# Optimization experiments

Measured on AMD Instinct MI355X. Metric: run time of the kernel, lower is better.

Reference implementation:

```python
import jax, jax.numpy as jnp
import numpy as np

HIDDEN = 2048
N_HEADS = 16
N_KV_HEADS = 8
HEAD_DIM = 128
ROTARY_DIM = 32  # int(128 * 0.25), already even
ROPE_THETA = 10000000.0
EPS = 1e-6
BATCH, SEQ = 2, 2048


def _rmsnorm(x, w, eps=EPS):
    # per-head RMSNorm over last dim; weight is zero-init, scale = 1 + w
    r = jax.lax.rsqrt(jnp.mean(x * x, axis=-1, keepdims=True) + eps)
    return x * r * (1.0 + w)


def _rope(x, positions, rotary_dim, theta):
    # x: [b, s, h, rotary_dim]; rotate-halves RoPE
    half = rotary_dim // 2
    inv_freq = 1.0 / (theta ** (jnp.arange(half, dtype=jnp.float32) / half))
    ang = positions.astype(jnp.float32)[:, :, None] * inv_freq  # [b, s, half]
    cos = jnp.cos(ang)[:, :, None, :]
    sin = jnp.sin(ang)[:, :, None, :]
    x1, x2 = x[..., :half], x[..., half:]
    return jnp.concatenate([x1 * cos - x2 * sin, x1 * sin + x2 * cos], axis=-1)


def setup_inputs() -> dict:
    key = jax.random.key(0)
    ks = jax.random.split(key, 8)
    scale = lambda fan_in: 1.0 / np.sqrt(fan_in)
    x = jax.random.normal(ks[0], (BATCH, SEQ, HIDDEN), dtype=jnp.float32)
    Wq = jax.random.normal(ks[1], (HIDDEN, N_HEADS * HEAD_DIM * 2), jnp.float32) * scale(HIDDEN)
    Wk = jax.random.normal(ks[2], (HIDDEN, N_KV_HEADS * HEAD_DIM), jnp.float32) * scale(HIDDEN)
    Wv = jax.random.normal(ks[3], (HIDDEN, N_KV_HEADS * HEAD_DIM), jnp.float32) * scale(HIDDEN)
    Wo = jax.random.normal(ks[4], (N_HEADS * HEAD_DIM, HIDDEN), jnp.float32) * scale(N_HEADS * HEAD_DIM)
    q_norm_w = jax.random.normal(ks[5], (HEAD_DIM,), jnp.float32) * 0.02
    k_norm_w = jax.random.normal(ks[6], (HEAD_DIM,), jnp.float32) * 0.02
    attention_mask = jnp.ones((BATCH, SEQ), dtype=jnp.int32)
    positions = jnp.broadcast_to(jnp.arange(SEQ, dtype=jnp.int32), (BATCH, SEQ))
    return {"x": x, "attention_mask": attention_mask, "positions": positions,
            "Wq": Wq, "Wk": Wk, "Wv": Wv, "Wo": Wo,
            "q_norm_w": q_norm_w, "k_norm_w": k_norm_w}


def reference(x, attention_mask, positions, Wq, Wk, Wv, Wo, q_norm_w, k_norm_w):
    b, s, _ = x.shape
    g = N_HEADS // N_KV_HEADS  # GQA group size

    q_all = jnp.einsum('bsh,ho->bso', x, Wq).reshape(b, s, N_HEADS, HEAD_DIM * 2)
    q, gate = jnp.split(q_all, 2, axis=-1)          # each [b,s,H,D]
    gate = gate.reshape(b, s, N_HEADS * HEAD_DIM)
    q = _rmsnorm(q, q_norm_w)
    k = _rmsnorm(jnp.einsum('bsh,ho->bso', x, Wk).reshape(b, s, N_KV_HEADS, HEAD_DIM), k_norm_w)
    v = jnp.einsum('bsh,ho->bso', x, Wv).reshape(b, s, N_KV_HEADS, HEAD_DIM)

    # partial RoPE on first ROTARY_DIM dims
    q = jnp.concatenate([_rope(q[..., :ROTARY_DIM], positions, ROTARY_DIM, ROPE_THETA), q[..., ROTARY_DIM:]], axis=-1)
    k = jnp.concatenate([_rope(k[..., :ROTARY_DIM], positions, ROTARY_DIM, ROPE_THETA), k[..., ROTARY_DIM:]], axis=-1)

    # grouped-query causal attention
    qg = q.reshape(b, s, N_KV_HEADS, g, HEAD_DIM)
    scores = jnp.einsum('bqhgd,bkhd->bhgqk', qg, k) / jnp.sqrt(jnp.float32(HEAD_DIM))
    causal = jnp.tril(jnp.ones((s, s), dtype=bool))
    key_valid = attention_mask.astype(bool)[:, None, None, None, :]  # [b,1,1,1,k]
    mask = causal[None, None, None, :, :] & key_valid
    scores = jnp.where(mask, scores, jnp.finfo(scores.dtype).min)
    probs = jax.nn.softmax(scores, axis=-1)
    attn = jnp.einsum('bhgqk,bkhd->bqhgd', probs, v).reshape(b, s, N_HEADS * HEAD_DIM)

    attn = attn * jax.nn.sigmoid(gate)
    return jnp.einsum('bso,oh->bsh', attn, Wo)
```

## Files before the change

### kernel.cpp

```cpp
#include <hip/hip_runtime.h>
#include <cstdint>

typedef __bf16  bf16;
typedef __bf16  bf16x8 __attribute__((ext_vector_type(8)));
typedef __bf16  bf16x4 __attribute__((ext_vector_type(4)));
typedef __bf16  bf16x2 __attribute__((ext_vector_type(2)));
typedef float   f32x4  __attribute__((ext_vector_type(4)));
typedef float   f32x16 __attribute__((ext_vector_type(16)));

#define GLOAD_LDS16(g, l) __builtin_amdgcn_global_load_lds( \
    (const __attribute__((address_space(1))) void*)(g),     \
    (__attribute__((address_space(3))) void*)(l), 16, 0, 0)

#define SEQ   2048
#define HID   2048
#define NH    16
#define NKV   8
#define HD    128
#define NQKV  6144
#define MTOT  4096

__device__ __forceinline__ void transw_body(const float* __restrict__ W, bf16* __restrict__ WT,
                                            int N, int n0, int k0, int t) {
    __shared__ float tile[64][65];
    int tn = t & 63, t4 = t >> 6;
    #pragma unroll
    for (int i = 0; i < 16; ++i) {
        int kk = i * 4 + t4;
        tile[kk][tn] = W[(size_t)(k0 + kk) * N + n0 + tn];
    }
    __syncthreads();
    #pragma unroll
    for (int i = 0; i < 16; ++i) {
        int nn = i * 4 + t4;
        WT[(size_t)(n0 + nn) * HID + k0 + tn] = (bf16)tile[tn][nn];
    }
}

__global__ __launch_bounds__(256) void prep_kernel(const float* __restrict__ x, bf16* __restrict__ xb,
                                                   const float* __restrict__ Wq, const float* __restrict__ Wk,
                                                   const float* __restrict__ Wv, const float* __restrict__ Wo,
                                                   bf16* __restrict__ wqkvT, bf16* __restrict__ woT) {
    int bx = blockIdx.x, t = threadIdx.x;
    if (bx < 8192) {
        int i = bx * 256 + t;
        f32x4 v = ((const f32x4*)x)[i];
        bf16x4 o;
        o[0] = (bf16)v[0]; o[1] = (bf16)v[1]; o[2] = (bf16)v[2]; o[3] = (bf16)v[3];
        ((bf16x4*)xb)[i] = o;
    } else if (bx < 8192 + 2048) {
        int idx = bx - 8192;
        transw_body(Wq, wqkvT, 4096, (idx & 63) * 64, (idx >> 6) * 64, t);
    } else if (bx < 8192 + 2048 + 512) {
        int idx = bx - (8192 + 2048);
        transw_body(Wk, wqkvT + (size_t)4096 * HID, 1024, (idx & 15) * 64, (idx >> 4) * 64, t);
    } else if (bx < 8192 + 2048 + 1024) {
        int idx = bx - (8192 + 2048 + 512);
        transw_body(Wv, wqkvT + (size_t)5120 * HID, 1024, (idx & 15) * 64, (idx >> 4) * 64, t);
    } else {
        int idx = bx - (8192 + 2048 + 1024);
        transw_body(Wo, woT, 2048, (idx & 31) * 64, (idx >> 5) * 64, t);
    }
}

template<bool OUT_BF16>
__global__ __launch_bounds__(256) void gemm_bt(const bf16* __restrict__ A, const bf16* __restrict__ Bt,
                                               void* __restrict__ C, int M, int N, int K) {
    __shared__ __align__(16) bf16 As[128 * 64];
    __shared__ __align__(16) bf16 Bs[128 * 64];
    const int tid = threadIdx.x;
    const int wave = tid >> 6, lane = tid & 63;
    const int l31 = lane & 31, half = lane >> 5;
    const int tile_n = blockIdx.x * 128, tile_m = blockIdx.y * 128;
    const int wm = (wave & 1) * 64, wn = (wave >> 1) * 64;
    const int sw = l31 & 7;
    f32x16 acc[2][2] = {};

    for (int k0 = 0; k0 < K; k0 += 64) {
        __syncthreads();
        #pragma unroll
        for (int j = 0; j < 4; ++j) {
            int s = j * 256 + tid;
            int row = s >> 3, c = s & 7;
            int cs = c ^ (row & 7);
            GLOAD_LDS16(A  + (size_t)(tile_m + row) * K + k0 + (cs << 3), As + (size_t)s * 8);
            GLOAD_LDS16(Bt + (size_t)(tile_n + row) * K + k0 + (cs << 3), Bs + (size_t)s * 8);
        }
        __syncthreads();
        #pragma unroll
        for (int ks = 0; ks < 4; ++ks) {
            int ch = ((ks * 2 + half) ^ sw) << 3;
            bf16x8 a0 = *(const bf16x8*)(As + (size_t)(wm + l31) * 64 + ch);
            bf16x8 a1 = *(const bf16x8*)(As + (size_t)(wm + 32 + l31) * 64 + ch);
            bf16x8 b0 = *(const bf16x8*)(Bs + (size_t)(wn + l31) * 64 + ch);
            bf16x8 b1 = *(const bf16x8*)(Bs + (size_t)(wn + 32 + l31) * 64 + ch);
            acc[0][0] = __builtin_amdgcn_mfma_f32_32x32x16_bf16(a0, b0, acc[0][0], 0, 0, 0);
            acc[0][1] = __builtin_amdgcn_mfma_f32_32x32x16_bf16(a0, b1, acc[0][1], 0, 0, 0);
            acc[1][0] = __builtin_amdgcn_mfma_f32_32x32x16_bf16(a1, b0, acc[1][0], 0, 0, 0);
            acc[1][1] = __builtin_amdgcn_mfma_f32_32x32x16_bf16(a1, b1, acc[1][1], 0, 0, 0);
        }
    }
    #pragma unroll
    for (int mt = 0; mt < 2; ++mt)
        #pragma unroll
        for (int nt = 0; nt < 2; ++nt)
            #pragma unroll
            for (int reg = 0; reg < 16; ++reg) {
                int row = tile_m + wm + mt * 32 + (reg & 3) + ((reg >> 2) * 8) + half * 4;
                int col = tile_n + wn + nt * 32 + l31;
                float v = acc[mt][nt][reg];
                if (OUT_BF16) ((bf16*)C)[(size_t)row * N + col] = (bf16)v;
                else          ((float*)C)[(size_t)row * N + col] = v;
            }
}

__global__ __launch_bounds__(256) void post_kernel(const bf16* __restrict__ qkv,
                                                   const float* __restrict__ qnw, const float* __restrict__ knw,
                                                   const int* __restrict__ positions,
                                                   bf16* __restrict__ Qh, bf16* __restrict__ Kh,
                                                   bf16* __restrict__ VT) {
    int bx = blockIdx.x;
    if (bx < 4096) {
        int tk = bx;
        int b = tk >> 11, s = tk & 2047;
        int wave = threadIdx.x >> 6, lane = threadIdx.x & 63;
        int e0 = lane * 2, e1 = e0 + 1;
        float pos = (float)positions[tk];
        const float L = 1.4533435415278355f;
        float a0 = pos * exp2f(-(float)(e0 & 15) * L);
        float a1 = pos * exp2f(-(float)(e1 & 15) * L);
        float cv0 = cosf(a0), sv0 = sinf(a0);
        float cv1 = cosf(a1), sv1 = sinf(a1);
        float qw0 = 1.0f + qnw[e0], qw1 = 1.0f + qnw[e1];
        float kw0 = 1.0f + knw[e0], kw1 = 1.0f + knw[e1];

        #pragma unroll
        for (int i = 0; i < 6; ++i) {
            bool isq = (i < 4);
            int h = wave + (isq ? i : (i - 4)) * 4;
            const bf16* base = qkv + (size_t)tk * NQKV + (isq ? h * 256 : 4096 + h * HD);
            bf16x2 v = *(const bf16x2*)(base + e0);
            float f0 = (float)v[0], f1 = (float)v[1];
            float ssq = f0 * f0 + f1 * f1;
            #pragma unroll
            for (int off = 32; off; off >>= 1) ssq += __shfl_xor(ssq, off);
            float rn = rsqrtf(ssq * (1.0f / 128.0f) + 1e-6f);
            float w0 = isq ? qw0 : kw0, w1 = isq ? qw1 : kw1;
            float x0 = f0 * rn * w0, x1 = f1 * rn * w1;
            float p0 = __shfl_xor(x0, 8), p1 = __shfl_xor(x1, 8);
            float r0 = x0, r1 = x1;
            if (lane < 8)       { r0 = x0 * cv0 - p0 * sv0; r1 = x1 * cv1 - p1 * sv1; }
            else if (lane < 16) { r0 = p0 * sv0 + x0 * cv0; r1 = p1 * sv1 + x1 * cv1; }
            bf16x2 o; o[0] = (bf16)r0; o[1] = (bf16)r1;
            bf16* dst = isq ? (Qh + ((size_t)(b * NH + h) * SEQ + s) * HD)
                            : (Kh + ((size_t)(b * NKV + h) * SEQ + s) * HD);
            *(bf16x2*)(dst + e0) = o;
        }
    } else {
        int idx = bx - 4096;
        int bh = idx >> 5, st = idx & 31;
        int b = bh >> 3, h = bh & 7;
        __shared__ float tile[64][129];
        int t = threadIdx.x;
        const bf16* src = qkv + ((size_t)(b * SEQ) + st * 64) * NQKV + 5120 + h * HD;
        #pragma unroll
        for (int i = 0; i < 32; ++i) {
            int ii = i * 256 + t;
            int tok = ii >> 7, d = ii & 127;
            tile[tok][d] = (float)src[(size_t)tok * NQKV + d];
        }
        __syncthreads();
        bf16* dst = VT + (size_t)(b * NKV + h) * HD * SEQ + st * 64;
        #pragma unroll
        for (int i = 0; i < 32; ++i) {
            int ii = i * 256 + t;
            int d = ii >> 6, sx = ii & 63;
            dst[(size_t)d * SEQ + sx] = (bf16)tile[sx][d];
        }
    }
}

__global__ __launch_bounds__(512, 4) void attn_kernel(const bf16* __restrict__ Qh, const bf16* __restrict__ Kh,
                                                      const bf16* __restrict__ VT, const bf16* __restrict__ qkv,
                                                      const int* __restrict__ amask, bf16* __restrict__ attnb) {
    const int bx = blockIdx.x;
    const int hb = (bx >> 4) & 31;
    const int head = hb & 15, b = hb >> 4;
    int q0 = ((bx & 15) + hb) & 15;
    const int qt = (bx & 256) ? (15 - q0) : q0;
    const int kvh = head >> 1;
    __shared__ __align__(16) bf16 Ks[2][64 * 128];
    __shared__ __align__(16) bf16 Vs[2][128 * 64];
    __shared__ __align__(16) bf16 Ps[8 * 16 * 64];
    const int tid = threadIdx.x, wave = tid >> 6, lane = tid & 63;
    const int quad = lane >> 4, cl = lane & 15;

    const bf16* qsrc = Qh + ((size_t)(b * NH + head) * SEQ + qt * 128) * HD;
    bf16x8 aq[4];
    #pragma unroll
    for (int kc = 0; kc < 4; ++kc)
        aq[kc] = *(const bf16x8*)(qsrc + (size_t)(wave * 16 + cl) * HD + kc * 32 + quad * 8);

    float lstate[4] = {0.0f, 0.0f, 0.0f, 0.0f};
    f32x4 oacc[8] = {};
    const int qrow_glob = qt * 128 + wave * 16 + quad * 4;
    const float scale = 0.08838834764831845f * 1.4426950408889634f;
    const float M = 20.0f;
    const int kmax = 2 * qt + 1;

    const bf16* kbase = Kh + (size_t)(b * NKV + kvh) * SEQ * HD;
    const bf16* vbase = VT + (size_t)(b * NKV + kvh) * HD * SEQ;

#define STAGE_KV(kt_, buf_) { \
    const bf16* ksrc = kbase + (size_t)(kt_) * 64 * HD; \
    const bf16* vsrc = vbase + (size_t)(kt_) * 64; \
    _Pragma("unroll") \
    for (int j = 0; j < 2; ++j) { \
        int s = j * 512 + tid;                     \
        int rK = s >> 4, cK = s & 15; \
        GLOAD_LDS16(ksrc + (size_t)rK * HD + ((cK ^ (rK & 15)) << 3), &Ks[buf_][0] + (size_t)s * 8); \
        int dV = s >> 3, cV = s & 7; \
        GLOAD_LDS16(vsrc + (size_t)dV * SEQ + ((cV ^ (dV & 7)) << 3), &Vs[buf_][0] + (size_t)s * 8); \
    } }

    STAGE_KV(0, 0);
    int cur = 0;
    for (int kt = 0; kt <= kmax; ++kt) {
        __syncthreads();
        if (kt < kmax) STAGE_KV(kt + 1, cur ^ 1);

        f32x4 sc[4] = {};
        #pragma unroll
        for (int nt = 0; nt < 4; ++nt)
            #pragma unroll
            for (int kc = 0; kc < 4; ++kc) {
                bf16x8 bk = *(const bf16x8*)(&Ks[cur][0] + (size_t)(nt * 16 + cl) * 128 + (((kc * 4 + quad) ^ cl) << 3));
                sc[nt] = __builtin_amdgcn_mfma_f32_16x16x32_bf16(aq[kc], bk, sc[nt], 0, 0, 0);
            }

        #pragma unroll
        for (int nt = 0; nt < 4; ++nt) {
            int kcol = kt * 64 + nt * 16 + cl;
            bool cok = (amask[b * SEQ + kcol] != 0);
            #pragma unroll
            for (int r = 0; r < 4; ++r) {
                bool ok = cok && (kcol <= qrow_glob + r);
                float p = ok ? exp2f(sc[nt][r] * scale - M) : 0.0f;
                lstate[r] += p;
                Ps[wave * 1024 + (quad * 4 + r) * 64 + ((nt * 16 + cl) ^ (quad << 4))] = (bf16)p;
            }
        }

        bf16x8 ap[2];
        #pragma unroll
        for (int c = 0; c < 2; ++c)
            ap[c] = *(const bf16x8*)(Ps + wave * 1024 + cl * 64 + ((c * 32 + quad * 8) ^ ((cl >> 2) << 4)));
        #pragma unroll
        for (int n2 = 0; n2 < 8; ++n2)
            #pragma unroll
            for (int c = 0; c < 2; ++c) {
                bf16x8 bv = *(const bf16x8*)(&Vs[cur][0] + (size_t)(n2 * 16 + cl) * 64 + (((c * 4 + quad) ^ (cl & 7)) << 3));
                oacc[n2] = __builtin_amdgcn_mfma_f32_16x16x32_bf16(ap[c], bv, oacc[n2], 0, 0, 0);
            }
        cur ^= 1;
    }
#undef STAGE_KV

    #pragma unroll
    for (int r = 0; r < 4; ++r) {
        #pragma unroll
        for (int off = 8; off; off >>= 1) lstate[r] += __shfl_xor(lstate[r], off);
        int srow = qt * 128 + wave * 16 + quad * 4 + r;
        float linv = 1.0f / lstate[r];
        #pragma unroll
        for (int n2 = 0; n2 < 8; ++n2) {
            int d = n2 * 16 + cl;
            float g = (float)qkv[(size_t)(b * SEQ + srow) * NQKV + head * 256 + 128 + d];
            float sig = 1.0f / (1.0f + __expf(-g));
            float v = oacc[n2][r] * linv * sig;
            attnb[(size_t)(b * SEQ + srow) * HID + head * HD + d] = (bf16)v;
        }
    }
}

extern "C" void kernel_launch(void* const* d_in, const int* in_sizes, int n_in,
                              void* d_out, int out_size, void* d_ws, size_t ws_size,
                              hipStream_t stream) {
    const float* x        = (const float*)d_in[0];
    const int*   amask    = (const int*)d_in[1];
    const int*   positions= (const int*)d_in[2];
    const float* Wq       = (const float*)d_in[3];
    const float* Wk       = (const float*)d_in[4];
    const float* Wv       = (const float*)d_in[5];
    const float* Wo       = (const float*)d_in[6];
    const float* qnw      = (const float*)d_in[7];
    const float* knw      = (const float*)d_in[8];
    float* out = (float*)d_out;
    char* ws = (char*)d_ws;

    bf16* xb    = (bf16*)(ws);
    bf16* wqkvT = (bf16*)(ws + 16777216);
    bf16* woT   = (bf16*)(ws + 41943040);
    bf16* qkv   = (bf16*)(ws + 50331648);
    bf16* Qh    = (bf16*)(ws + 100663296);
    bf16* Kh    = (bf16*)(ws + 117440512);
    bf16* VT    = (bf16*)(ws + 125829120);
    bf16* attnb = (bf16*)(ws + 134217728);

    prep_kernel<<<12288, 256, 0, stream>>>(x, xb, Wq, Wk, Wv, Wo, wqkvT, woT);
    gemm_bt<true><<<dim3(48, 32), 256, 0, stream>>>(xb, wqkvT, qkv, MTOT, NQKV, HID);
    post_kernel<<<4608, 256, 0, stream>>>(qkv, qnw, knw, positions, Qh, Kh, VT);
    attn_kernel<<<512, 512, 0, stream>>>(Qh, Kh, VT, qkv, amask, attnb);
    gemm_bt<false><<<dim3(16, 32), 256, 0, stream>>>(attnb, woT, out, MTOT, HID, HID);

    (void)in_sizes; (void)n_in; (void)out_size; (void)ws_size;
}
```

Baseline: 390.5 us.

## Vectorize prep/post memory accesses and ballot the attention mask per tile

The weight transpose now writes 16-byte bf16x8 vectors instead of scalar bf16 stores. The x conversion handles eight elements per thread with half the blocks. The post kernel processes eight elements per lane and reads the norm weights as vectors, computing RoPE sin/cos only on rotary lanes. The attention kernel loads the mask once per key tile and distributes it with a ballot, replacing a per-column global load. These cut instruction count and memory transactions in the bandwidth-bound auxiliary kernels, at the cost of more LDS bank conflicts in the strided transpose reads.

```diff
diff --git a/kernel.cpp b/kernel.cpp
--- a/kernel.cpp
+++ b/kernel.cpp
@@ -30,10 +30,15 @@
         tile[kk][tn] = W[(size_t)(k0 + kk) * N + n0 + tn];
     }
     __syncthreads();
-    #pragma unroll
-    for (int i = 0; i < 16; ++i) {
-        int nn = i * 4 + t4;
-        WT[(size_t)(n0 + nn) * HID + k0 + tn] = (bf16)tile[tn][nn];
+    int tk8 = (t & 7) * 8;
+    int tnn = t >> 3;
+    #pragma unroll
+    for (int i = 0; i < 2; ++i) {
+        int nn = i * 32 + tnn;
+        bf16x8 o;
+        #pragma unroll
+        for (int j = 0; j < 8; ++j) o[j] = (bf16)tile[tk8 + j][nn];
+        *(bf16x8*)(&WT[(size_t)(n0 + nn) * HID + k0 + tk8]) = o;
     }
 }
 
@@ -42,23 +47,25 @@
                                                    const float* __restrict__ Wv, const float* __restrict__ Wo,
                                                    bf16* __restrict__ wqkvT, bf16* __restrict__ woT) {
     int bx = blockIdx.x, t = threadIdx.x;
-    if (bx < 8192) {
+    if (bx < 4096) {
         int i = bx * 256 + t;
-        f32x4 v = ((const f32x4*)x)[i];
-        bf16x4 o;
-        o[0] = (bf16)v[0]; o[1] = (bf16)v[1]; o[2] = (bf16)v[2]; o[3] = (bf16)v[3];
-        ((bf16x4*)xb)[i] = o;
-    } else if (bx < 8192 + 2048) {
-        int idx = bx - 8192;
+        f32x4 v0 = ((const f32x4*)x)[i * 2];
+        f32x4 v1 = ((const f32x4*)x)[i * 2 + 1];
+        bf16x8 o;
+        o[0] = (bf16)v0[0]; o[1] = (bf16)v0[1]; o[2] = (bf16)v0[2]; o[3] = (bf16)v0[3];
+        o[4] = (bf16)v1[0]; o[5] = (bf16)v1[1]; o[6] = (bf16)v1[2]; o[7] = (bf16)v1[3];
+        ((bf16x8*)xb)[i] = o;
+    } else if (bx < 4096 + 2048) {
+        int idx = bx - 4096;
         transw_body(Wq, wqkvT, 4096, (idx & 63) * 64, (idx >> 6) * 64, t);
-    } else if (bx < 8192 + 2048 + 512) {
-        int idx = bx - (8192 + 2048);
+    } else if (bx < 4096 + 2048 + 512) {
+        int idx = bx - (4096 + 2048);
         transw_body(Wk, wqkvT + (size_t)4096 * HID, 1024, (idx & 15) * 64, (idx >> 4) * 64, t);
-    } else if (bx < 8192 + 2048 + 1024) {
-        int idx = bx - (8192 + 2048 + 512);
+    } else if (bx < 4096 + 2048 + 1024) {
+        int idx = bx - (4096 + 2048 + 512);
         transw_body(Wv, wqkvT + (size_t)5120 * HID, 1024, (idx & 15) * 64, (idx >> 4) * 64, t);
     } else {
-        int idx = bx - (8192 + 2048 + 1024);
+        int idx = bx - (4096 + 2048 + 1024);
         transw_body(Wo, woT, 2048, (idx & 31) * 64, (idx >> 5) * 64, t);
     }
 }
@@ -124,37 +131,59 @@
         int tk = bx;
         int b = tk >> 11, s = tk & 2047;
         int wave = threadIdx.x >> 6, lane = threadIdx.x & 63;
-        int e0 = lane * 2, e1 = e0 + 1;
+        int g16 = lane >> 4;
+        int l16 = lane & 15;
+        int d0 = l16 * 8;
         float pos = (float)positions[tk];
         const float L = 1.4533435415278355f;
-        float a0 = pos * exp2f(-(float)(e0 & 15) * L);
-        float a1 = pos * exp2f(-(float)(e1 & 15) * L);
-        float cv0 = cosf(a0), sv0 = sinf(a0);
-        float cv1 = cosf(a1), sv1 = sinf(a1);
-        float qw0 = 1.0f + qnw[e0], qw1 = 1.0f + qnw[e1];
-        float kw0 = 1.0f + knw[e0], kw1 = 1.0f + knw[e1];
-
-        #pragma unroll
-        for (int i = 0; i < 6; ++i) {
-            bool isq = (i < 4);
-            int h = wave + (isq ? i : (i - 4)) * 4;
-            const bf16* base = qkv + (size_t)tk * NQKV + (isq ? h * 256 : 4096 + h * HD);
-            bf16x2 v = *(const bf16x2*)(base + e0);
-            float f0 = (float)v[0], f1 = (float)v[1];
-            float ssq = f0 * f0 + f1 * f1;
-            #pragma unroll
-            for (int off = 32; off; off >>= 1) ssq += __shfl_xor(ssq, off);
+
+        float cv[8], sv[8];
+        if (l16 < 4) {
+            #pragma unroll
+            for (int j = 0; j < 8; ++j) {
+                float a = pos * exp2f(-(float)((l16 & 1) * 8 + j) * L);
+                cv[j] = cosf(a); sv[j] = sinf(a);
+            }
+        }
+
+        #pragma unroll
+        for (int i = 0; i < 2; ++i) {
+            int slot = i * 16 + wave * 4 + g16;
+            if (slot >= 24) continue;
+            bool isq = (slot < 16);
+            int h = isq ? slot : slot - 16;
+            const bf16* base = qkv + (size_t)tk * NQKV + (isq ? h * 256 : 4096 + h * HD) + d0;
+            bf16x8 v = *(const bf16x8*)base;
+            float f[8];
+            float ssq = 0.0f;
+            #pragma unroll
+            for (int j = 0; j < 8; ++j) { f[j] = (float)v[j]; ssq += f[j] * f[j]; }
+            #pragma unroll
+            for (int off = 8; off; off >>= 1) ssq += __shfl_xor(ssq, off);
             float rn = rsqrtf(ssq * (1.0f / 128.0f) + 1e-6f);
-            float w0 = isq ? qw0 : kw0, w1 = isq ? qw1 : kw1;
-            float x0 = f0 * rn * w0, x1 = f1 * rn * w1;
-            float p0 = __shfl_xor(x0, 8), p1 = __shfl_xor(x1, 8);
-            float r0 = x0, r1 = x1;
-            if (lane < 8)       { r0 = x0 * cv0 - p0 * sv0; r1 = x1 * cv1 - p1 * sv1; }
-            else if (lane < 16) { r0 = p0 * sv0 + x0 * cv0; r1 = p1 * sv1 + x1 * cv1; }
-            bf16x2 o; o[0] = (bf16)r0; o[1] = (bf16)r1;
+            const float* nw = isq ? qnw : knw;
+            f32x4 wa = *(const f32x4*)(nw + d0);
+            f32x4 wb = *(const f32x4*)(nw + d0 + 4);
+            float xv[8];
+            #pragma unroll
+            for (int j = 0; j < 4; ++j) { xv[j] = f[j] * rn * (1.0f + wa[j]); xv[j + 4] = f[j + 4] * rn * (1.0f + wb[j]); }
+            float out[8];
+            #pragma unroll
+            for (int j = 0; j < 8; ++j) out[j] = xv[j];
+            if (l16 < 4) {
+                #pragma unroll
+                for (int j = 0; j < 8; ++j) {
+                    float p = __shfl_xor(xv[j], 2);
+                    out[j] = (l16 < 2) ? (xv[j] * cv[j] - p * sv[j])
+                                       : (xv[j] * cv[j] + p * sv[j]);
+                }
+            }
+            bf16x8 o;
+            #pragma unroll
+            for (int j = 0; j < 8; ++j) o[j] = (bf16)out[j];
             bf16* dst = isq ? (Qh + ((size_t)(b * NH + h) * SEQ + s) * HD)
                             : (Kh + ((size_t)(b * NKV + h) * SEQ + s) * HD);
-            *(bf16x2*)(dst + e0) = o;
+            *(bf16x8*)(dst + d0) = o;
         }
     } else {
         int idx = bx - 4096;
@@ -227,6 +256,7 @@
     int cur = 0;
     for (int kt = 0; kt <= kmax; ++kt) {
         __syncthreads();
+        int mv = amask[b * SEQ + kt * 64 + lane];
         if (kt < kmax) STAGE_KV(kt + 1, cur ^ 1);
 
         f32x4 sc[4] = {};
@@ -238,10 +268,11 @@
                 sc[nt] = __builtin_amdgcn_mfma_f32_16x16x32_bf16(aq[kc], bk, sc[nt], 0, 0, 0);
             }
 
+        unsigned long long mbits = __ballot(mv != 0);
         #pragma unroll
         for (int nt = 0; nt < 4; ++nt) {
             int kcol = kt * 64 + nt * 16 + cl;
-            bool cok = (amask[b * SEQ + kcol] != 0);
+            bool cok = (mbits >> (nt * 16 + cl)) & 1ull;
             #pragma unroll
             for (int r = 0; r < 4; ++r) {
                 bool ok = cok && (kcol <= qrow_glob + r);
@@ -307,7 +338,7 @@
     bf16* VT    = (bf16*)(ws + 125829120);
     bf16* attnb = (bf16*)(ws + 134217728);
 
-    prep_kernel<<<12288, 256, 0, stream>>>(x, xb, Wq, Wk, Wv, Wo, wqkvT, woT);
+    prep_kernel<<<8192, 256, 0, stream>>>(x, xb, Wq, Wk, Wv, Wo, wqkvT, woT);
     gemm_bt<true><<<dim3(48, 32), 256, 0, stream>>>(xb, wqkvT, qkv, MTOT, NQKV, HID);
     post_kernel<<<4608, 256, 0, stream>>>(qkv, qnw, knw, positions, Qh, Kh, VT);
     attn_kernel<<<512, 512, 0, stream>>>(Qh, Kh, VT, qkv, amask, attnb);
```

New measurement: 399.8 us. 2.4% more time.
